# Optimization experiments

Measured on AMD Instinct MI355X. Metric: run time of the kernel, lower is better.

## Reference

```python
import jax, jax.numpy as jnp
import numpy as np

N_PATCHES = 14  # per side -> 196 patches

def patchify(images, n_patches):
    # images: [n, c, h, w]; returns [n, n_patches**2, c*ps*ps] with flatten order (c, ph, pw)
    n, c, h, w = images.shape
    ps = h // n_patches
    x = images.reshape(n, c, n_patches, ps, n_patches, ps)
    x = x.transpose(0, 2, 4, 1, 3, 5)  # [n, np_i, np_j, c, ps, ps]
    return x.reshape(n, n_patches * n_patches, c * ps * ps)

def setup_inputs() -> dict:
    key = jax.random.key(0)
    k1, k2, k3, k4 = jax.random.split(key, 4)
    B, C, H, Wd = 64, 3, 224, 224
    input_d = C * (H // N_PATCHES) * (Wd // N_PATCHES)  # 768
    hidden_d = 768
    images = jax.random.normal(k1, (B, C, H, Wd), dtype=jnp.float32)
    W = jax.random.normal(k2, (hidden_d, input_d), dtype=jnp.float32) * (1.0 / np.sqrt(input_d))
    b = jax.random.normal(k3, (hidden_d,), dtype=jnp.float32) * 0.01
    class_token = jax.random.uniform(k4, (1, hidden_d), dtype=jnp.float32)
    return {"images": images, "W": W, "b": b, "class_token": class_token}

def reference(images, W, b, class_token):
    patches = patchify(images, N_PATCHES)               # [B, 196, 768]
    tokens = jnp.einsum('bpd,hd->bph', patches, W) + b  # linear_mapper
    B = tokens.shape[0]
    cls = jnp.broadcast_to(class_token[None, :, :], (B, 1, class_token.shape[-1]))
    return jnp.concatenate([cls, tokens], axis=1)       # [B, 197, hidden_d]
```

## Files before the change

kernel.cpp:

```cpp
#include <hip/hip_runtime.h>
#include <cstdint>
#include <cstddef>

#define MTOT 12544
#define KTOT 768
#define NTOT 768

typedef float  f32x4  __attribute__((ext_vector_type(4)));
typedef __bf16 bf16x8 __attribute__((ext_vector_type(8)));

#define IMG_ELEMS (64*3*224*224)
#define W_ELEMS   (768*768)
#define A_BLOCKS  (IMG_ELEMS/8/256)
#define W_BLOCKS  (W_ELEMS/8/256)
#define CLS_BLOCKS 48

__global__ __launch_bounds__(256) void prep_kernel(
    const float* __restrict__ images, const float* __restrict__ Wm,
    const float* __restrict__ cls, float* __restrict__ out,
    __bf16* __restrict__ imgb, __bf16* __restrict__ Wb) {
  const int bid = blockIdx.x, tid = threadIdx.x;
  if (bid < A_BLOCKS) {
    const size_t q = (size_t)bid * 256 + tid;
    const float4 v0 = *(const float4*)(images + q * 8);
    const float4 v1 = *(const float4*)(images + q * 8 + 4);
    bf16x8 o;
    o[0]=(__bf16)v0.x; o[1]=(__bf16)v0.y; o[2]=(__bf16)v0.z; o[3]=(__bf16)v0.w;
    o[4]=(__bf16)v1.x; o[5]=(__bf16)v1.y; o[6]=(__bf16)v1.z; o[7]=(__bf16)v1.w;
    *(bf16x8*)(imgb + q * 8) = o;
  } else if (bid < A_BLOCKS + W_BLOCKS) {
    const size_t q = (size_t)(bid - A_BLOCKS) * 256 + tid;
    const float4 v0 = *(const float4*)(Wm + q * 8);
    const float4 v1 = *(const float4*)(Wm + q * 8 + 4);
    bf16x8 o;
    o[0]=(__bf16)v0.x; o[1]=(__bf16)v0.y; o[2]=(__bf16)v0.z; o[3]=(__bf16)v0.w;
    o[4]=(__bf16)v1.x; o[5]=(__bf16)v1.y; o[6]=(__bf16)v1.z; o[7]=(__bf16)v1.w;
    *(bf16x8*)(Wb + q * 8) = o;
  } else {
    const int t  = (bid - A_BLOCKS - W_BLOCKS) * 256 + tid;
    const int bb = t / 192;
    const int r  = t - bb * 192;
    *(float4*)(out + (size_t)bb * 197 * 768 + r * 4) = *(const float4*)(cls + r * 4);
  }
}

#define BM 64
#define BN 128
#define BK 64
#define NBLK_N 6

__device__ __forceinline__ void gload_lds16(const void* g, void* l) {
  __builtin_amdgcn_global_load_lds((__attribute__((address_space(1))) void*)(g),
                                   (__attribute__((address_space(3))) void*)(l),
                                   16, 0, 0);
}

__global__ __launch_bounds__(256) void gemm_kernel(
    const __bf16* __restrict__ imgb, const __bf16* __restrict__ Wb,
    const float* __restrict__ bias, float* __restrict__ out) {
  __shared__ __bf16 As[2 * 64 * 32];
  __shared__ __bf16 Bs[2 * 128 * 32];

  const int tid  = threadIdx.x;
  const int bx   = blockIdx.x;
  const int mblk = bx / NBLK_N;
  const int nblk = bx - mblk * NBLK_N;
  const int m0 = mblk * BM;
  const int n0 = nblk * BN;
  const int wave = tid >> 6, lane = tid & 63;
  const int wm = (wave & 1) * 32;
  const int wn = (wave >> 1) * 64;
  const int lrow = lane & 15, lq = lane >> 4;

  f32x4 acc[2][4] = {};

  const __bf16* pA[2];
#pragma unroll
  for (int s = 0; s < 2; ++s) {
    const int c = wave * 128 + s * 64 + lane;
    const int kstep = c >> 8, rem = c & 255;
    const int row = rem >> 2, jc = rem & 3;
    const int m = m0 + row;
    const int bb = m / 196, p = m - bb * 196;
    const int pi = p / 14, pj = p - pi * 14;
    const int ph_off = kstep * 2 + (jc >> 1);
    const int pw_off = (jc & 1) * 8;
    const size_t e = ((size_t)(bb * 3 * 224 + pi * 16 + ph_off)) * 224 + pj * 16 + pw_off;
    pA[s] = imgb + e;
  }
  const __bf16* pB[4];
#pragma unroll
  for (int s = 0; s < 4; ++s) {
    const int c = wave * 256 + s * 64 + lane;
    const int kstep = c >> 9, rem = c & 511;
    const int h = rem >> 2, jc = rem & 3;
    pB[s] = Wb + (size_t)(n0 + h) * 768 + kstep * 32 + jc * 8;
  }
  __bf16* lA[2];
  __bf16* lB[4];
#pragma unroll
  for (int s = 0; s < 2; ++s) lA[s] = As + (wave * 128 + s * 64) * 8;
#pragma unroll
  for (int s = 0; s < 4; ++s) lB[s] = Bs + (wave * 256 + s * 64) * 8;

  for (int kt = 0; kt < KTOT / BK; ++kt) {
#pragma unroll
    for (int s = 0; s < 2; ++s) gload_lds16(pA[s], lA[s]);
#pragma unroll
    for (int s = 0; s < 4; ++s) gload_lds16(pB[s], lB[s]);
    const int dA = ((kt & 3) == 3) ? 47488 : 896;
    pA[0] += dA; pA[1] += dA;
    pB[0] += BK; pB[1] += BK; pB[2] += BK; pB[3] += BK;
    __syncthreads();

#pragma unroll
    for (int ks = 0; ks < 2; ++ks) {
      bf16x8 af[2], bf[4];
#pragma unroll
      for (int i = 0; i < 2; ++i)
        af[i] = *(const bf16x8*)&As[ks * 2048 + (wm + i * 16 + lrow) * 32 + lq * 8];
#pragma unroll
      for (int j = 0; j < 4; ++j)
        bf[j] = *(const bf16x8*)&Bs[ks * 4096 + (wn + j * 16 + lrow) * 32 + lq * 8];
#pragma unroll
      for (int i = 0; i < 2; ++i)
#pragma unroll
        for (int j = 0; j < 4; ++j)
          acc[i][j] = __builtin_amdgcn_mfma_f32_16x16x32_bf16(af[i], bf[j], acc[i][j], 0, 0, 0);
    }
    __syncthreads();
  }

#pragma unroll
  for (int j = 0; j < 4; ++j) {
    const int h  = n0 + wn + j * 16 + lrow;
    const float bv = bias[h];
#pragma unroll
    for (int i = 0; i < 2; ++i) {
      const int mb = m0 + wm + i * 16 + lq * 4;
#pragma unroll
      for (int r = 0; r < 4; ++r) {
        const int m  = mb + r;
        const int bb = m / 196, p = m - bb * 196;
        out[(size_t)(bb * 197 + 1 + p) * 768 + h] = acc[i][j][r] + bv;
      }
    }
  }
}

extern "C" void kernel_launch(void* const* d_in, const int* in_sizes, int n_in,
                              void* d_out, int out_size, void* d_ws, size_t ws_size,
                              hipStream_t stream) {
  const float* images = (const float*)d_in[0];
  const float* Wm     = (const float*)d_in[1];
  const float* b      = (const float*)d_in[2];
  const float* cls    = (const float*)d_in[3];
  float* out = (float*)d_out;

  __bf16* imgb = (__bf16*)d_ws;
  __bf16* Wb   = imgb + (size_t)IMG_ELEMS;
  (void)in_sizes; (void)n_in; (void)out_size; (void)ws_size;

  prep_kernel<<<A_BLOCKS + W_BLOCKS + CLS_BLOCKS, 256, 0, stream>>>(
      images, Wm, cls, out, imgb, Wb);
  gemm_kernel<<<(MTOT / BM) * NBLK_N, 256, 0, stream>>>(imgb, Wb, b, out);
}
```

Before: 117.3 us.

## Fuse bf16 conversion into GEMM with register-prefetched fp32 loads and larger tile

Removes the separate prep kernel that converted images and weights to bf16 in a workspace. The GEMM now loads fp32 directly into registers one K-step ahead, converts to bf16 and writes to LDS, which also handles the patchify gather. The M tile grows from 64 to 128 and block ordering becomes M-major within each N column. This removes a kernel launch and the workspace round trip, but each block re-reads fp32 inputs that are twice the size of bf16 and carries more register pressure.

After: 148.7 us. +26.8%, slower.

```diff
diff --git a/kernel.cpp b/kernel.cpp
--- a/kernel.cpp
+++ b/kernel.cpp
@@ -6,124 +6,114 @@
 #define KTOT 768
 #define NTOT 768
 
+#define BM 128
+#define BN 128
+#define BK 64
+#define NBLK_M 98
+#define NBLK_N 6
+#define CLS_BLOCKS 48
+
 typedef float  f32x4  __attribute__((ext_vector_type(4)));
 typedef __bf16 bf16x8 __attribute__((ext_vector_type(8)));
 
-#define IMG_ELEMS (64*3*224*224)
-#define W_ELEMS   (768*768)
-#define A_BLOCKS  (IMG_ELEMS/8/256)
-#define W_BLOCKS  (W_ELEMS/8/256)
-#define CLS_BLOCKS 48
+__device__ __forceinline__ void cvt16_write(const float4* r, __bf16* dst) {
+  bf16x8 o0, o1;
+  o0[0]=(__bf16)r[0].x; o0[1]=(__bf16)r[0].y; o0[2]=(__bf16)r[0].z; o0[3]=(__bf16)r[0].w;
+  o0[4]=(__bf16)r[1].x; o0[5]=(__bf16)r[1].y; o0[6]=(__bf16)r[1].z; o0[7]=(__bf16)r[1].w;
+  o1[0]=(__bf16)r[2].x; o1[1]=(__bf16)r[2].y; o1[2]=(__bf16)r[2].z; o1[3]=(__bf16)r[2].w;
+  o1[4]=(__bf16)r[3].x; o1[5]=(__bf16)r[3].y; o1[6]=(__bf16)r[3].z; o1[7]=(__bf16)r[3].w;
+  *(bf16x8*)(dst)     = o0;
+  *(bf16x8*)(dst + 8) = o1;
+}
 
-__global__ __launch_bounds__(256) void prep_kernel(
+__global__ __launch_bounds__(256) void fused_kernel(
     const float* __restrict__ images, const float* __restrict__ Wm,
-    const float* __restrict__ cls, float* __restrict__ out,
-    __bf16* __restrict__ imgb, __bf16* __restrict__ Wb) {
-  const int bid = blockIdx.x, tid = threadIdx.x;
-  if (bid < A_BLOCKS) {
-    const size_t q = (size_t)bid * 256 + tid;
-    const float4 v0 = *(const float4*)(images + q * 8);
-    const float4 v1 = *(const float4*)(images + q * 8 + 4);
-    bf16x8 o;
-    o[0]=(__bf16)v0.x; o[1]=(__bf16)v0.y; o[2]=(__bf16)v0.z; o[3]=(__bf16)v0.w;
-    o[4]=(__bf16)v1.x; o[5]=(__bf16)v1.y; o[6]=(__bf16)v1.z; o[7]=(__bf16)v1.w;
-    *(bf16x8*)(imgb + q * 8) = o;
-  } else if (bid < A_BLOCKS + W_BLOCKS) {
-    const size_t q = (size_t)(bid - A_BLOCKS) * 256 + tid;
-    const float4 v0 = *(const float4*)(Wm + q * 8);
-    const float4 v1 = *(const float4*)(Wm + q * 8 + 4);
-    bf16x8 o;
-    o[0]=(__bf16)v0.x; o[1]=(__bf16)v0.y; o[2]=(__bf16)v0.z; o[3]=(__bf16)v0.w;
-    o[4]=(__bf16)v1.x; o[5]=(__bf16)v1.y; o[6]=(__bf16)v1.z; o[7]=(__bf16)v1.w;
-    *(bf16x8*)(Wb + q * 8) = o;
-  } else {
-    const int t  = (bid - A_BLOCKS - W_BLOCKS) * 256 + tid;
-    const int bb = t / 192;
-    const int r  = t - bb * 192;
+    const float* __restrict__ bias, const float* __restrict__ cls,
+    float* __restrict__ out) {
+  __shared__ __bf16 As[2 * 128 * 32];
+  __shared__ __bf16 Bs[2 * 128 * 32];
+
+  const int tid = threadIdx.x;
+  const int bx  = blockIdx.x;
+
+  if (bx < CLS_BLOCKS) {
+    const int t  = bx * 256 + tid;
+    const int bb = t / 192, r = t - bb * 192;
     *(float4*)(out + (size_t)bb * 197 * 768 + r * 4) = *(const float4*)(cls + r * 4);
   }
-}
 
-#define BM 64
-#define BN 128
-#define BK 64
-#define NBLK_N 6
-
-__device__ __forceinline__ void gload_lds16(const void* g, void* l) {
-  __builtin_amdgcn_global_load_lds((__attribute__((address_space(1))) void*)(g),
-                                   (__attribute__((address_space(3))) void*)(l),
-                                   16, 0, 0);
-}
-
-__global__ __launch_bounds__(256) void gemm_kernel(
-    const __bf16* __restrict__ imgb, const __bf16* __restrict__ Wb,
-    const float* __restrict__ bias, float* __restrict__ out) {
-  __shared__ __bf16 As[2 * 64 * 32];
-  __shared__ __bf16 Bs[2 * 128 * 32];
-
-  const int tid  = threadIdx.x;
-  const int bx   = blockIdx.x;
-  const int mblk = bx / NBLK_N;
-  const int nblk = bx - mblk * NBLK_N;
-  const int m0 = mblk * BM;
-  const int n0 = nblk * BN;
+  const int mblk = bx % NBLK_M;
+  const int nblk = bx / NBLK_M;
+  const int m0 = mblk * BM, n0 = nblk * BN;
   const int wave = tid >> 6, lane = tid & 63;
-  const int wm = (wave & 1) * 32;
+  const int wm = (wave & 1) * 64;
   const int wn = (wave >> 1) * 64;
   const int lrow = lane & 15, lq = lane >> 4;
 
-  f32x4 acc[2][4] = {};
-
-  const __bf16* pA[2];
+  const float* pA[2];
+  __bf16* lA[2];
 #pragma unroll
   for (int s = 0; s < 2; ++s) {
-    const int c = wave * 128 + s * 64 + lane;
-    const int kstep = c >> 8, rem = c & 255;
-    const int row = rem >> 2, jc = rem & 3;
+    const int unit = s * 256 + tid;
+    const int row = unit & 127, jc = unit >> 7;
     const int m = m0 + row;
     const int bb = m / 196, p = m - bb * 196;
     const int pi = p / 14, pj = p - pi * 14;
-    const int ph_off = kstep * 2 + (jc >> 1);
-    const int pw_off = (jc & 1) * 8;
-    const size_t e = ((size_t)(bb * 3 * 224 + pi * 16 + ph_off)) * 224 + pj * 16 + pw_off;
-    pA[s] = imgb + e;
+    pA[s] = images + ((size_t)(bb * 3 * 224) + pi * 16 + jc) * 224 + pj * 16;
+    lA[s] = As + (jc >> 1) * 4096 + row * 32 + (jc & 1) * 16;
   }
-  const __bf16* pB[4];
+  const float* pB[2];
+  __bf16* lB[2];
 #pragma unroll
-  for (int s = 0; s < 4; ++s) {
-    const int c = wave * 256 + s * 64 + lane;
-    const int kstep = c >> 9, rem = c & 511;
-    const int h = rem >> 2, jc = rem & 3;
-    pB[s] = Wb + (size_t)(n0 + h) * 768 + kstep * 32 + jc * 8;
+  for (int s = 0; s < 2; ++s) {
+    const int hrow = (tid >> 2) + s * 64;
+    const int jc = tid & 3;
+    pB[s] = Wm + (size_t)(n0 + hrow) * 768 + jc * 16;
+    lB[s] = Bs + (jc >> 1) * 4096 + hrow * 32 + (jc & 1) * 16;
   }
-  __bf16* lA[2];
-  __bf16* lB[4];
+
+  f32x4 acc[4][4] = {};
+  float4 ra[2][4], rb[2][4];
+
 #pragma unroll
-  for (int s = 0; s < 2; ++s) lA[s] = As + (wave * 128 + s * 64) * 8;
+  for (int s = 0; s < 2; ++s)
 #pragma unroll
-  for (int s = 0; s < 4; ++s) lB[s] = Bs + (wave * 256 + s * 64) * 8;
+    for (int q = 0; q < 4; ++q) {
+      ra[s][q] = *(const float4*)(pA[s] + q * 4);
+      rb[s][q] = *(const float4*)(pB[s] + q * 4);
+    }
 
   for (int kt = 0; kt < KTOT / BK; ++kt) {
 #pragma unroll
-    for (int s = 0; s < 2; ++s) gload_lds16(pA[s], lA[s]);
+    for (int s = 0; s < 2; ++s) {
+      cvt16_write(ra[s], lA[s]);
+      cvt16_write(rb[s], lB[s]);
+    }
+    __syncthreads();
+
+    const int dA = ((kt & 3) == 3) ? 47488 : 896;
+    pA[0] += dA; pA[1] += dA; pB[0] += BK; pB[1] += BK;
+    if (kt < KTOT / BK - 1) {
 #pragma unroll
-    for (int s = 0; s < 4; ++s) gload_lds16(pB[s], lB[s]);
-    const int dA = ((kt & 3) == 3) ? 47488 : 896;
-    pA[0] += dA; pA[1] += dA;
-    pB[0] += BK; pB[1] += BK; pB[2] += BK; pB[3] += BK;
-    __syncthreads();
+      for (int s = 0; s < 2; ++s)
+#pragma unroll
+        for (int q = 0; q < 4; ++q) {
+          ra[s][q] = *(const float4*)(pA[s] + q * 4);
+          rb[s][q] = *(const float4*)(pB[s] + q * 4);
+        }
+    }
 
 #pragma unroll
     for (int ks = 0; ks < 2; ++ks) {
-      bf16x8 af[2], bf[4];
+      bf16x8 af[4], bf[4];
 #pragma unroll
-      for (int i = 0; i < 2; ++i)
-        af[i] = *(const bf16x8*)&As[ks * 2048 + (wm + i * 16 + lrow) * 32 + lq * 8];
+      for (int i = 0; i < 4; ++i)
+        af[i] = *(const bf16x8*)&As[ks * 4096 + (wm + i * 16 + lrow) * 32 + lq * 8];
 #pragma unroll
       for (int j = 0; j < 4; ++j)
         bf[j] = *(const bf16x8*)&Bs[ks * 4096 + (wn + j * 16 + lrow) * 32 + lq * 8];
 #pragma unroll
-      for (int i = 0; i < 2; ++i)
+      for (int i = 0; i < 4; ++i)
 #pragma unroll
         for (int j = 0; j < 4; ++j)
           acc[i][j] = __builtin_amdgcn_mfma_f32_16x16x32_bf16(af[i], bf[j], acc[i][j], 0, 0, 0);
@@ -136,7 +126,7 @@
     const int h  = n0 + wn + j * 16 + lrow;
     const float bv = bias[h];
 #pragma unroll
-    for (int i = 0; i < 2; ++i) {
+    for (int i = 0; i < 4; ++i) {
       const int mb = m0 + wm + i * 16 + lq * 4;
 #pragma unroll
       for (int r = 0; r < 4; ++r) {
@@ -156,12 +146,7 @@
   const float* b      = (const float*)d_in[2];
   const float* cls    = (const float*)d_in[3];
   float* out = (float*)d_out;
+  (void)in_sizes; (void)n_in; (void)out_size; (void)d_ws; (void)ws_size;
 
-  __bf16* imgb = (__bf16*)d_ws;
-  __bf16* Wb   = imgb + (size_t)IMG_ELEMS;
-  (void)in_sizes; (void)n_in; (void)out_size; (void)ws_size;
-
-  prep_kernel<<<A_BLOCKS + W_BLOCKS + CLS_BLOCKS, 256, 0, stream>>>(
-      images, Wm, cls, out, imgb, Wb);
-  gemm_kernel<<<(MTOT / BM) * NBLK_N, 256, 0, stream>>>(imgb, Wb, b, out);
+  fused_kernel<<<NBLK_M * NBLK_N, 256, 0, stream>>>(images, Wm, b, cls, out);
 }
```
